# Kernel optimization log

Measured on AMD Instinct MI355X. Metric: run time of the kernel, lower is better.

The kernel has to match this reference:

```python
import jax, jax.numpy as jnp
import numpy as np

# Fixed hyperparameters matching init_kwargs
DIL_START = 2
DIL_END = 1024   # n_dilations = 1022
N_BULGE = 2
BATCH, L, C = 8, 2048, 4


def _variant_tables():
    """Static (forward_shift, backward_shift, has_GU) table, one row per output feature.
    Order per distance s: [main AU_CG+GU, left bulge d=1..n, right bulge d=1..n]."""
    f, b, g = [], [], []
    for s in range(DIL_START, DIL_END):
        f.append(s + 1); b.append(s + 1); g.append(1.0)            # dilate
        for d in range(1, N_BULGE + 1):                            # left bulge
            f.append(s + 1); b.append(s + 1 + d); g.append(0.0)
        for d in range(1, N_BULGE + 1):                            # right bulge
            f.append(s + 1 + d); b.append(s + 1); g.append(0.0)
    return np.array(f), np.array(b), np.array(g, dtype=np.float32)


def setup_inputs() -> dict:
    key = jax.random.key(0)
    x = jax.random.uniform(key, (BATCH, L, C), dtype=jnp.float32)
    return {"x": x}


def reference(x) -> jnp.ndarray:
    n, L_, _ = x.shape
    f_np, b_np, g_np = _variant_tables()
    f_arr = jnp.asarray(f_np)
    b_arr = jnp.asarray(b_np)
    gu_arr = jnp.asarray(g_np).astype(x.dtype)
    max_f = int(f_np.max())
    max_b = int(b_np.max())

    # y[i] = x[i+f] (zeros past the end);  z[i] = x[i-b] (zeros before start)
    xp_r = jnp.pad(x, ((0, 0), (0, max_f), (0, 0)))
    xp_l = jnp.pad(x, ((0, 0), (max_b, 0), (0, 0)))
    w4 = jnp.array([2.0, 3.0, 3.0, 2.0], dtype=x.dtype)  # AU/CG pairing weights

    def variant(f, b, g):
        y = jax.lax.dynamic_slice_in_dim(xp_r, f, L_, axis=1)          # (n, L, 4)
        z = jax.lax.dynamic_slice_in_dim(xp_l, max_b - b, L_, axis=1)  # (n, L, 4)
        # base: sum_c w[c] * x[i+f, c] * x[i-b, 3-c]  (reverse-complement correlation)
        base = jnp.einsum('nlc,nlc->nl', y * w4, z[..., ::-1])
        # GU wobble pairs (channels 2,3), weight 2, only for the non-bulge variant
        gu = 2.0 * (y[..., 2] * z[..., 3] + y[..., 3] * z[..., 2])
        return base + g * gu

    out = jax.vmap(variant)(f_arr, b_arr, gu_arr)  # (F, n, L)
    return jnp.transpose(out, (1, 2, 0))           # (n, L, F)
```

## Files before the change

kernel.cpp:

```cpp
#include <hip/hip_runtime.h>

#define LSEQ 2048
#define NS   1022
#define NF   5110
#define NB   8
#define IT   128
#define GI   4
#define TPB  256
#define FPB  (TPB * 5)

__device__ __forceinline__ float4 zero4() { return make_float4(0.f, 0.f, 0.f, 0.f); }

__device__ __forceinline__ float basescore(const float4 y, const float4 z) {
    return 2.f * y.x * z.w + 3.f * y.y * z.z + 3.f * y.z * z.y + 2.f * y.w * z.x;
}

__global__ __launch_bounds__(TPB) void fdcnn_kernel(const float4* __restrict__ x,
                                                    float* __restrict__ out) {
    __shared__ float4 xs[LSEQ];
    __shared__ float st[GI][FPB];

    const int t = threadIdx.x;
    const int n = blockIdx.z;
    const float4* xg = x + (size_t)n * LSEQ;
    #pragma unroll
    for (int k = 0; k < LSEQ / TPB; ++k)
        xs[t + k * TPB] = xg[t + k * TPB];
    __syncthreads();

    const int sidx = blockIdx.x * TPB + t;
    const int s = sidx + 2;
    const int i0 = blockIdx.y * IT;
    const int fbase = blockIdx.x * FPB;

    float4 yA, yB, zA, zB;
    {
        int p = i0 + s + 1;
        yA = xs[p & (LSEQ - 1)]; if (p >= LSEQ) yA = zero4();
        p = i0 + s + 2;
        yB = xs[p & (LSEQ - 1)]; if (p >= LSEQ) yB = zero4();
        int q = i0 - s - 3;
        zA = xs[q & (LSEQ - 1)]; if (q < 0) zA = zero4();
        q = i0 - s - 2;
        zB = xs[q & (LSEQ - 1)]; if (q < 0) zB = zero4();
    }

    for (int gb = 0; gb < IT / GI; ++gb) {
        #pragma unroll
        for (int ig = 0; ig < GI; ++ig) {
            const int i = i0 + gb * GI + ig;

            int p = i + s + 3;
            float4 yC = xs[p & (LSEQ - 1)]; if (p >= LSEQ) yC = zero4();
            int q = i - s - 1;
            float4 zC = xs[q & (LSEQ - 1)]; if (q < 0) zC = zero4();

            const float4 y1 = yA, y2 = yB, y3 = yC;
            const float4 z3 = zA, z2 = zB, z1 = zC;

            float* sp = &st[ig][t * 5];
            sp[0] = basescore(y1, z1) + 2.f * (y1.z * z1.w + y1.w * z1.z);
            sp[1] = basescore(y1, z2);
            sp[2] = basescore(y1, z3);
            sp[3] = basescore(y2, z1);
            sp[4] = basescore(y3, z1);

            yA = yB; yB = yC;
            zA = zB; zB = zC;
        }
        __syncthreads();

        const size_t obase = ((size_t)n * LSEQ + (i0 + gb * GI)) * (size_t)NF;
        #pragma unroll
        for (int k = 0; k < 5; ++k) {
            const int v  = k * TPB + t;
            const int ig = v / 320;
            const int fo = (v - ig * 320) * 4;
            const int rem = NF - (fbase + fo);
            const float4 val = *(const float4*)&st[ig][fo];
            float* dst = out + obase + (size_t)ig * NF + fbase + fo;
            if (rem >= 4) {
                *(float4*)dst = val;
            } else if (rem > 0) {
                dst[0] = val.x;
                if (rem > 1) dst[1] = val.y;
            }
        }
        __syncthreads();
    }
}

extern "C" void kernel_launch(void* const* d_in, const int* in_sizes, int n_in,
                              void* d_out, int out_size, void* d_ws, size_t ws_size,
                              hipStream_t stream) {
    const float4* x = (const float4*)d_in[0];
    float* out = (float*)d_out;
    dim3 grid((NS + TPB - 1) / TPB, LSEQ / IT, NB);
    dim3 block(TPB);
    fdcnn_kernel<<<grid, block, 0, stream>>>(x, out);
}
```

Before: 72.81 us.

## Double-buffer staging tile, read x from global, halve rows per block

The shared-memory copy of the input sequence is removed, and each thread now reads x directly from global memory (cached) with clamped indices. The staging buffer is double-buffered so computing the next group of rows overlaps with writing out the current one, using one raw barrier per group instead of two syncthreads. Rows per block drop from 128 to 64, doubling the grid for more parallelism. The cost is more global and L1 traffic for x loads and twice the per-block setup. Correctness depends on the hand-written s_waitcnt plus barrier ordering.

```diff
diff --git a/kernel.cpp b/kernel.cpp
--- a/kernel.cpp
+++ b/kernel.cpp
@@ -4,81 +4,78 @@
 #define NS   1022
 #define NF   5110
 #define NB   8
-#define IT   128
+#define IT   64
 #define GI   4
+#define NGRP (IT / GI)
 #define TPB  256
 #define FPB  (TPB * 5)
-
-__device__ __forceinline__ float4 zero4() { return make_float4(0.f, 0.f, 0.f, 0.f); }
 
 __device__ __forceinline__ float basescore(const float4 y, const float4 z) {
     return 2.f * y.x * z.w + 3.f * y.y * z.z + 3.f * y.z * z.y + 2.f * y.w * z.x;
 }
 
+__device__ __forceinline__ float4 loadx(const float4* __restrict__ xg, int p) {
+    int pc = p < 0 ? 0 : (p > LSEQ - 1 ? LSEQ - 1 : p);
+    float4 v = xg[pc];
+    if ((unsigned)p >= (unsigned)LSEQ) v = make_float4(0.f, 0.f, 0.f, 0.f);
+    return v;
+}
+
 __global__ __launch_bounds__(TPB) void fdcnn_kernel(const float4* __restrict__ x,
                                                     float* __restrict__ out) {
-    __shared__ float4 xs[LSEQ];
-    __shared__ float st[GI][FPB];
+    __shared__ float st[2][GI][FPB];
 
     const int t = threadIdx.x;
     const int n = blockIdx.z;
     const float4* xg = x + (size_t)n * LSEQ;
-    #pragma unroll
-    for (int k = 0; k < LSEQ / TPB; ++k)
-        xs[t + k * TPB] = xg[t + k * TPB];
-    __syncthreads();
 
     const int sidx = blockIdx.x * TPB + t;
     const int s = sidx + 2;
     const int i0 = blockIdx.y * IT;
     const int fbase = blockIdx.x * FPB;
 
-    float4 yA, yB, zA, zB;
-    {
-        int p = i0 + s + 1;
-        yA = xs[p & (LSEQ - 1)]; if (p >= LSEQ) yA = zero4();
-        p = i0 + s + 2;
-        yB = xs[p & (LSEQ - 1)]; if (p >= LSEQ) yB = zero4();
-        int q = i0 - s - 3;
-        zA = xs[q & (LSEQ - 1)]; if (q < 0) zA = zero4();
-        q = i0 - s - 2;
-        zB = xs[q & (LSEQ - 1)]; if (q < 0) zB = zero4();
-    }
+    float4 yA = loadx(xg, i0 + s + 1);
+    float4 yB = loadx(xg, i0 + s + 2);
+    float4 zA = loadx(xg, i0 - s - 3);
+    float4 zB = loadx(xg, i0 - s - 2);
 
-    for (int gb = 0; gb < IT / GI; ++gb) {
+    auto compute_group = [&](int g) {
+        float* stg = &st[g & 1][0][0];
         #pragma unroll
         for (int ig = 0; ig < GI; ++ig) {
-            const int i = i0 + gb * GI + ig;
-
-            int p = i + s + 3;
-            float4 yC = xs[p & (LSEQ - 1)]; if (p >= LSEQ) yC = zero4();
-            int q = i - s - 1;
-            float4 zC = xs[q & (LSEQ - 1)]; if (q < 0) zC = zero4();
-
+            const int i = i0 + g * GI + ig;
+            float4 yC = loadx(xg, i + s + 3);
+            float4 zC = loadx(xg, i - s - 1);
             const float4 y1 = yA, y2 = yB, y3 = yC;
             const float4 z3 = zA, z2 = zB, z1 = zC;
-
-            float* sp = &st[ig][t * 5];
+            float* sp = stg + ig * FPB + t * 5;
             sp[0] = basescore(y1, z1) + 2.f * (y1.z * z1.w + y1.w * z1.z);
             sp[1] = basescore(y1, z2);
             sp[2] = basescore(y1, z3);
             sp[3] = basescore(y2, z1);
             sp[4] = basescore(y3, z1);
-
             yA = yB; yB = yC;
             zA = zB; zB = zC;
         }
-        __syncthreads();
+    };
 
-        const size_t obase = ((size_t)n * LSEQ + (i0 + gb * GI)) * (size_t)NF;
+    compute_group(0);
+
+    for (int g = 0; g < NGRP; ++g) {
+        asm volatile("s_waitcnt lgkmcnt(0)\n\ts_barrier" ::: "memory");
+
+        if (g + 1 < NGRP) compute_group(g + 1);
+
+        const float* stg = &st[g & 1][0][0];
+        float* obase = out + ((size_t)n * LSEQ + (i0 + g * GI)) * (size_t)NF + fbase;
         #pragma unroll
         for (int k = 0; k < 5; ++k) {
             const int v  = k * TPB + t;
             const int ig = v / 320;
             const int fo = (v - ig * 320) * 4;
             const int rem = NF - (fbase + fo);
-            const float4 val = *(const float4*)&st[ig][fo];
-            float* dst = out + obase + (size_t)ig * NF + fbase + fo;
+            const float4 val = *(const float4*)(stg + ig * FPB + fo);
+            float* dst = obase + (size_t)ig * NF + fo;
             if (rem >= 4) {
                 *(float4*)dst = val;
             } else if (rem > 0) {
@@ -86,7 +83,6 @@
                 if (rem > 1) dst[1] = val.y;
             }
         }
-        __syncthreads();
     }
 }
 
```

After: 76.83 us. 1.06x slower.
